# Kernel optimization log

Hardware: AMD Instinct MI355X
Metric: run time of the kernel (lower is better)

Reference implementation:

```python
import jax, jax.numpy as jnp
import numpy as np

EPS = 1e-5

def _conv1x1(x, w):
    # x: (B, Cin, N, K), w: (Cout, Cin) -> (B, Cout, N, K)
    return jnp.einsum('oc,bcnk->bonk', w, x)

def _bn2d(x, gamma, beta):
    # eval-mode BN with running_mean=0, running_var=1 (fresh init)
    scale = gamma / jnp.sqrt(1.0 + EPS)
    return x * scale[None, :, None, None] + beta[None, :, None, None]

def setup_inputs() -> dict:
    key = jax.random.key(0)
    ks = jax.random.split(key, 10)
    B, Cin, N, K = 8, 64, 1024, 32
    Cout, M = 64, 8
    Cin2 = 2 * Cin  # kernel_input='w_neighbor'
    features = jax.random.normal(ks[0], (B, Cin, N, K), dtype=jnp.float32)
    points_xyz = jax.random.normal(ks[1], (B, 3, N, K), dtype=jnp.float32)
    # ScoreNet convs: mlp_channels [7,16,16,16,M]; first 3 have BN (no bias), last has bias
    w1 = jax.random.normal(ks[2], (16, 7), dtype=jnp.float32) * (2.0 / 7) ** 0.5
    w2 = jax.random.normal(ks[3], (16, 16), dtype=jnp.float32) * (2.0 / 16) ** 0.5
    w3 = jax.random.normal(ks[4], (16, 16), dtype=jnp.float32) * (2.0 / 16) ** 0.5
    w4 = jax.random.normal(ks[5], (M, 16), dtype=jnp.float32) * (2.0 / 16) ** 0.5
    b4 = jnp.zeros((M,), dtype=jnp.float32)
    g1 = jnp.ones((16,), jnp.float32); be1 = jnp.zeros((16,), jnp.float32)
    g2 = jnp.ones((16,), jnp.float32); be2 = jnp.zeros((16,), jnp.float32)
    g3 = jnp.ones((16,), jnp.float32); be3 = jnp.zeros((16,), jnp.float32)
    # weight bank: kaiming_normal on (M, 2Cin, Cout) -> stored as (2Cin, M, Cout)
    wb = jax.random.normal(ks[6], (Cin2, M, Cout), dtype=jnp.float32) * (2.0 / Cin2) ** 0.5
    bn_g = jnp.ones((Cout,), jnp.float32); bn_b = jnp.zeros((Cout,), jnp.float32)
    return dict(features=features, points_xyz=points_xyz,
                w1=w1, g1=g1, be1=be1, w2=w2, g2=g2, be2=be2,
                w3=w3, g3=g3, be3=be3, w4=w4, b4=b4,
                weight_bank=wb, bn_g=bn_g, bn_b=bn_b)

def reference(features, points_xyz, w1, g1, be1, w2, g2, be2, w3, g3, be3,
              w4, b4, weight_bank, bn_g, bn_b):
    B, Cin, N, K = features.shape
    M = weight_bank.shape[1]
    # kernel_input = 'w_neighbor': concat(feat - center, feat) -> (B, 2Cin, N, K)
    center_f = features[..., :1]
    feat = jnp.concatenate([features - center_f, features], axis=1)
    # scorenet input = 'w_neighbor_dist': (center_xyz, xyz_diff, dist) -> (B, 7, N, K)
    center_xyz = jnp.broadcast_to(points_xyz[..., :1], points_xyz.shape)
    xyz_diff = points_xyz - center_xyz
    dist = jnp.sqrt(jnp.sum(xyz_diff * xyz_diff, axis=1, keepdims=True))
    xyz_feats = jnp.concatenate([center_xyz, xyz_diff, dist], axis=1)
    h = jax.nn.relu(_bn2d(_conv1x1(xyz_feats, w1), g1, be1))
    h = jax.nn.relu(_bn2d(_conv1x1(h, w2), g2, be2))
    h = jax.nn.relu(_bn2d(_conv1x1(h, w3), g3, be3))
    s = _conv1x1(h, w4) + b4[None, :, None, None]  # (B, M, N, K)
    scores = jax.nn.softmax(s, axis=1)
    scores = jnp.transpose(scores, (0, 2, 3, 1))  # (B, N, K, M)
    # matmul with weight bank then score-weighted sum over kernels, fused via einsum
    # original: (B,N,K,2Cin)@(2Cin,M*Cout) -> (B,N,K,M,Cout); sum_m scores * . -> (B,N,K,Cout)
    new_features = jnp.einsum('bcnk,cmo,bnkm->bonk', feat, weight_bank, scores)
    # BN2d (eval, fresh stats) + ReLU
    new_features = jax.nn.relu(_bn2d(new_features, bn_g, bn_b))
    return new_features
```

## Files before the change

### kernel.cpp

```cpp
#include <hip/hip_runtime.h>
#include <hip/hip_bf16.h>

typedef __attribute__((ext_vector_type(8))) short bf16x8;
typedef __attribute__((ext_vector_type(4))) float f32x4;
typedef __attribute__((ext_vector_type(2))) float f32x2;

#define BNSCL 0.9999950000375f

__global__ __launch_bounds__(256) void k_prep_wbt(const float* __restrict__ wb,
                                                  __hip_bfloat16* __restrict__ wbt)
{
    int idx = blockIdx.x * 256 + threadIdx.x;
    int o = idx >> 10;
    int cm = idx & 1023;
    wbt[idx] = __float2bfloat16(wb[cm * 64 + o]);
}

__global__ __launch_bounds__(256) void k_scores(
    const float* __restrict__ xyz,
    const float* __restrict__ w1, const float* __restrict__ g1, const float* __restrict__ be1,
    const float* __restrict__ w2, const float* __restrict__ g2, const float* __restrict__ be2,
    const float* __restrict__ w3, const float* __restrict__ g3, const float* __restrict__ be3,
    const float* __restrict__ w4, const float* __restrict__ b4,
    float* __restrict__ scores)
{
    __shared__ float lw[856];
    const int tid = threadIdx.x;
    if (tid < 112) lw[tid] = w1[tid];
    lw[112 + tid] = w2[tid];
    lw[368 + tid] = w3[tid];
    if (tid < 128) lw[624 + tid] = w4[tid];
    if (tid < 8)   lw[752 + tid] = b4[tid];
    if (tid < 16) {
        lw[760 + tid] = g1[tid] * BNSCL;  lw[776 + tid] = be1[tid];
        lw[792 + tid] = g2[tid] * BNSCL;  lw[808 + tid] = be2[tid];
        lw[824 + tid] = g3[tid] * BNSCL;  lw[840 + tid] = be3[tid];
    }
    __syncthreads();

    float in7[2][7], h1[2][16], h2[2][16], s[2][8];

#pragma unroll
    for (int q = 0; q < 2; ++q) {
        int g = blockIdx.x * 512 + q * 256 + tid;
        int b = g >> 15;
        int p = g & 32767;
        int pc = p & ~31;
        const float* xb = xyz + (size_t)b * 98304;
        float cx = xb[pc], cy = xb[32768 + pc], cz = xb[65536 + pc];
        float dx = xb[p] - cx, dy = xb[32768 + p] - cy, dz = xb[65536 + p] - cz;
        in7[q][0] = cx; in7[q][1] = cy; in7[q][2] = cz;
        in7[q][3] = dx; in7[q][4] = dy; in7[q][5] = dz;
        in7[q][6] = sqrtf(dx * dx + dy * dy + dz * dz);
    }

#pragma unroll
    for (int o = 0; o < 16; ++o) {
        float a0 = 0.f, a1 = 0.f;
#pragma unroll
        for (int c = 0; c < 7; ++c) {
            float w = lw[o * 7 + c];
            a0 += w * in7[0][c]; a1 += w * in7[1][c];
        }
        float gs = lw[760 + o], bb = lw[776 + o];
        h1[0][o] = fmaxf(a0 * gs + bb, 0.f);
        h1[1][o] = fmaxf(a1 * gs + bb, 0.f);
    }
#pragma unroll
    for (int o = 0; o < 16; ++o) {
        float a0 = 0.f, a1 = 0.f;
#pragma unroll
        for (int c = 0; c < 16; ++c) {
            float w = lw[112 + o * 16 + c];
            a0 += w * h1[0][c]; a1 += w * h1[1][c];
        }
        float gs = lw[792 + o], bb = lw[808 + o];
        h2[0][o] = fmaxf(a0 * gs + bb, 0.f);
        h2[1][o] = fmaxf(a1 * gs + bb, 0.f);
    }
#pragma unroll
    for (int o = 0; o < 16; ++o) {
        float a0 = 0.f, a1 = 0.f;
#pragma unroll
        for (int c = 0; c < 16; ++c) {
            float w = lw[368 + o * 16 + c];
            a0 += w * h2[0][c]; a1 += w * h2[1][c];
        }
        float gs = lw[824 + o], bb = lw[840 + o];
        h1[0][o] = fmaxf(a0 * gs + bb, 0.f);
        h1[1][o] = fmaxf(a1 * gs + bb, 0.f);
    }
#pragma unroll
    for (int o = 0; o < 8; ++o) {
        float bb = lw[752 + o];
        float a0 = bb, a1 = bb;
#pragma unroll
        for (int c = 0; c < 16; ++c) {
            float w = lw[624 + o * 16 + c];
            a0 += w * h1[0][c]; a1 += w * h1[1][c];
        }
        s[0][o] = a0; s[1][o] = a1;
    }

#pragma unroll
    for (int q = 0; q < 2; ++q) {
        int g = blockIdx.x * 512 + q * 256 + tid;
        float mx = s[q][0];
#pragma unroll
        for (int i = 1; i < 8; ++i) mx = fmaxf(mx, s[q][i]);
        float sum = 0.f;
#pragma unroll
        for (int i = 0; i < 8; ++i) { s[q][i] = __expf(s[q][i] - mx); sum += s[q][i]; }
        float inv = 1.f / sum;
        float4 lo = {s[q][0] * inv, s[q][1] * inv, s[q][2] * inv, s[q][3] * inv};
        float4 hi = {s[q][4] * inv, s[q][5] * inv, s[q][6] * inv, s[q][7] * inv};
        *(float4*)(scores + (size_t)g * 8) = lo;
        *(float4*)(scores + (size_t)g * 8 + 4) = hi;
    }
}

__global__ __launch_bounds__(512, 8) void k_main(
    const float* __restrict__ feat,
    const float* __restrict__ scores,
    const __hip_bfloat16* __restrict__ wbt,
    const float* __restrict__ bn_g, const float* __restrict__ bn_b,
    float* __restrict__ out)
{
    __shared__ __align__(16) short lwb[64 * 256];

    const int tid  = threadIdx.x;
    const int lane = tid & 63;
    const int wave = tid >> 6;
    const int col  = lane & 15;
    const int row4 = lane >> 4;

    const int pblock = blockIdx.x * 128;
    const int b    = pblock >> 15;
    const int pl0  = pblock & 32767;
    const int pcol = pl0 + wave * 16 + col;
    const int pcen = __builtin_amdgcn_readfirstlane(pcol & ~31);
    const int gp   = pblock + wave * 16 + col;

    const float* fb = feat + (size_t)b * 2097152;

    const float* sp = scores + (size_t)gp * 8;
    f32x2 s01 = *(const f32x2*)sp;
    f32x2 s23 = *(const f32x2*)(sp + 2);
    f32x2 s45 = *(const f32x2*)(sp + 4);
    f32x2 s67 = *(const f32x2*)(sp + 6);

    f32x4 acc[4];
#pragma unroll
    for (int i = 0; i < 4; ++i) { f32x4 z = {0.f, 0.f, 0.f, 0.f}; acc[i] = z; }

    const ushort* wsrc = (const ushort*)wbt;

#pragma unroll
    for (int phase = 0; phase < 4; ++phase) {
#pragma unroll
        for (int it = 0; it < 4; ++it) {
            int chunk = it * 512 + tid;
            int o = chunk >> 5, c8 = chunk & 31;
            int4 v = *(const int4*)(wsrc + (o << 10) + (phase << 8) + (c8 << 3));
            *(int4*)&lwb[(o << 8) + (((c8 ^ o) & 31) << 3)] = v;
        }
        __syncthreads();

#pragma unroll 4
        for (int kk = 0; kk < 8; ++kk) {
            int cp = phase * 32 + kk * 4 + row4;
            float fv;
            if (phase < 2) {
                const float* fpc = fb + (size_t)cp * 32768;
                fv = fpc[pcol] - fpc[pcen];
            } else {
                fv = fb[(size_t)(cp - 64) * 32768 + pcol];
            }

            f32x2 fvv = {fv, fv};
            f32x2 p0 = fvv * s01, p1 = fvv * s23, p2 = fvv * s45, p3 = fvv * s67;
            int4 bi;
            { __hip_bfloat162 q = __float22bfloat162_rn(make_float2(p0.x, p0.y)); __builtin_memcpy(&bi.x, &q, 4); }
            { __hip_bfloat162 q = __float22bfloat162_rn(make_float2(p1.x, p1.y)); __builtin_memcpy(&bi.y, &q, 4); }
            { __hip_bfloat162 q = __float22bfloat162_rn(make_float2(p2.x, p2.y)); __builtin_memcpy(&bi.z, &q, 4); }
            { __hip_bfloat162 q = __float22bfloat162_rn(make_float2(p3.x, p3.y)); __builtin_memcpy(&bi.w, &q, 4); }
            bf16x8 bv = __builtin_bit_cast(bf16x8, bi);

            int bcm = kk * 4 + row4;
#pragma unroll
            for (int ot = 0; ot < 4; ++ot) {
                int o = ot * 16 + col;
                bf16x8 af = *(const bf16x8*)&lwb[(o << 8) + (((bcm ^ o) & 31) << 3)];
                acc[ot] = __builtin_amdgcn_mfma_f32_16x16x32_bf16(af, bv, acc[ot], 0, 0, 0);
            }
        }
        __syncthreads();
    }

#pragma unroll
    for (int ot = 0; ot < 4; ++ot) {
#pragma unroll
        for (int r = 0; r < 4; ++r) {
            int o = ot * 16 + row4 * 4 + r;
            float v = acc[ot][r];
            v = v * (bn_g[o] * BNSCL) + bn_b[o];
            v = fmaxf(v, 0.f);
            out[((size_t)(b * 64 + o) << 15) + pcol] = v;
        }
    }
}

extern "C" void kernel_launch(void* const* d_in, const int* in_sizes, int n_in,
                              void* d_out, int out_size, void* d_ws, size_t ws_size,
                              hipStream_t stream)
{
    const float* features = (const float*)d_in[0];
    const float* xyz      = (const float*)d_in[1];
    const float* w1  = (const float*)d_in[2];
    const float* g1  = (const float*)d_in[3];
    const float* be1 = (const float*)d_in[4];
    const float* w2  = (const float*)d_in[5];
    const float* g2  = (const float*)d_in[6];
    const float* be2 = (const float*)d_in[7];
    const float* w3  = (const float*)d_in[8];
    const float* g3  = (const float*)d_in[9];
    const float* be3 = (const float*)d_in[10];
    const float* w4  = (const float*)d_in[11];
    const float* b4  = (const float*)d_in[12];
    const float* wb  = (const float*)d_in[13];
    const float* bn_g = (const float*)d_in[14];
    const float* bn_b = (const float*)d_in[15];

    float* scores = (float*)d_ws;
    __hip_bfloat16* wbt = (__hip_bfloat16*)((char*)d_ws + 8388608);

    k_prep_wbt<<<256, 256, 0, stream>>>(wb, wbt);
    k_scores<<<512, 256, 0, stream>>>(xyz, w1, g1, be1, w2, g2, be2,
                                      w3, g3, be3, w4, b4, scores);
    k_main<<<2048, 512, 0, stream>>>(features, scores, wbt, bn_g, bn_b,
                                     (float*)d_out);
}
```

Before: 199.0 us.

## Switch main GEMM to 32x32x16 MFMA with two point tiles per wave; fuse weight prep

```diff
diff --git a/kernel.cpp b/kernel.cpp
--- a/kernel.cpp
+++ b/kernel.cpp
@@ -2,19 +2,9 @@
 #include <hip/hip_bf16.h>
 
 typedef __attribute__((ext_vector_type(8))) short bf16x8;
-typedef __attribute__((ext_vector_type(4))) float f32x4;
-typedef __attribute__((ext_vector_type(2))) float f32x2;
+typedef __attribute__((ext_vector_type(16))) float f32x16;
 
 #define BNSCL 0.9999950000375f
-
-__global__ __launch_bounds__(256) void k_prep_wbt(const float* __restrict__ wb,
-                                                  __hip_bfloat16* __restrict__ wbt)
-{
-    int idx = blockIdx.x * 256 + threadIdx.x;
-    int o = idx >> 10;
-    int cm = idx & 1023;
-    wbt[idx] = __float2bfloat16(wb[cm * 64 + o]);
-}
 
 __global__ __launch_bounds__(256) void k_scores(
     const float* __restrict__ xyz,
@@ -22,10 +12,18 @@
     const float* __restrict__ w2, const float* __restrict__ g2, const float* __restrict__ be2,
     const float* __restrict__ w3, const float* __restrict__ g3, const float* __restrict__ be3,
     const float* __restrict__ w4, const float* __restrict__ b4,
+    const float* __restrict__ wb, __hip_bfloat16* __restrict__ wbt,
     float* __restrict__ scores)
 {
     __shared__ float lw[856];
     const int tid = threadIdx.x;
+
+    if (blockIdx.x < 256) {
+        int idx = blockIdx.x * 256 + tid;
+        int o = idx >> 10, cm = idx & 1023;
+        wbt[idx] = __float2bfloat16(wb[cm * 64 + o]);
+    }
+
     if (tid < 112) lw[tid] = w1[tid];
     lw[112 + tid] = w2[tid];
     lw[368 + tid] = w3[tid];
@@ -119,7 +117,7 @@
     }
 }
 
-__global__ __launch_bounds__(512, 8) void k_main(
+__global__ __launch_bounds__(256, 4) void k_main(
     const float* __restrict__ feat,
     const float* __restrict__ scores,
     const __hip_bfloat16* __restrict__ wbt,
@@ -131,81 +129,97 @@
     const int tid  = threadIdx.x;
     const int lane = tid & 63;
     const int wave = tid >> 6;
-    const int col  = lane & 15;
-    const int row4 = lane >> 4;
-
-    const int pblock = blockIdx.x * 128;
+    const int l31  = lane & 31;
+    const int lh   = lane >> 5;
+
+    const int pblock = blockIdx.x * 256;
     const int b    = pblock >> 15;
     const int pl0  = pblock & 32767;
-    const int pcol = pl0 + wave * 16 + col;
-    const int pcen = __builtin_amdgcn_readfirstlane(pcol & ~31);
-    const int gp   = pblock + wave * 16 + col;
+
+    const int ptl0 = pl0 + (wave * 2 + 0) * 32;
+    const int ptl1 = pl0 + (wave * 2 + 1) * 32;
+    const int pc0  = ptl0 + l31;
+    const int pc1  = ptl1 + l31;
 
     const float* fb = feat + (size_t)b * 2097152;
 
-    const float* sp = scores + (size_t)gp * 8;
-    f32x2 s01 = *(const f32x2*)sp;
-    f32x2 s23 = *(const f32x2*)(sp + 2);
-    f32x2 s45 = *(const f32x2*)(sp + 4);
-    f32x2 s67 = *(const f32x2*)(sp + 6);
-
-    f32x4 acc[4];
-#pragma unroll
-    for (int i = 0; i < 4; ++i) { f32x4 z = {0.f, 0.f, 0.f, 0.f}; acc[i] = z; }
+    const float* sp0 = scores + ((size_t)(pblock + (wave * 2) * 32 + l31)) * 8;
+    const float* sp1 = sp0 + 256;
+    float4 s0lo = *(const float4*)sp0, s0hi = *(const float4*)(sp0 + 4);
+    float4 s1lo = *(const float4*)sp1, s1hi = *(const float4*)(sp1 + 4);
+
+    f32x16 acc[2][2];
+#pragma unroll
+    for (int q = 0; q < 2; ++q)
+#pragma unroll
+        for (int ot = 0; ot < 2; ++ot) {
+            f32x16 z = {0.f,0.f,0.f,0.f,0.f,0.f,0.f,0.f,0.f,0.f,0.f,0.f,0.f,0.f,0.f,0.f};
+            acc[q][ot] = z;
+        }
 
     const ushort* wsrc = (const ushort*)wbt;
 
 #pragma unroll
     for (int phase = 0; phase < 4; ++phase) {
 #pragma unroll
-        for (int it = 0; it < 4; ++it) {
-            int chunk = it * 512 + tid;
+        for (int it = 0; it < 8; ++it) {
+            int chunk = it * 256 + tid;
             int o = chunk >> 5, c8 = chunk & 31;
             int4 v = *(const int4*)(wsrc + (o << 10) + (phase << 8) + (c8 << 3));
-            *(int4*)&lwb[(o << 8) + (((c8 ^ o) & 31) << 3)] = v;
+            *(int4*)&lwb[(o << 8) + (((c8 ^ (o & 31)) & 31) << 3)] = v;
         }
         __syncthreads();
 
 #pragma unroll 4
-        for (int kk = 0; kk < 8; ++kk) {
-            int cp = phase * 32 + kk * 4 + row4;
-            float fv;
+        for (int kk = 0; kk < 16; ++kk) {
+            int cr = ((phase & 1) << 5) + kk * 2 + lh;
+            const float* fr = fb + ((size_t)cr << 15);
+            float fv0, fv1;
             if (phase < 2) {
-                const float* fpc = fb + (size_t)cp * 32768;
-                fv = fpc[pcol] - fpc[pcen];
+                fv0 = fr[pc0] - fr[ptl0];
+                fv1 = fr[pc1] - fr[ptl1];
             } else {
-                fv = fb[(size_t)(cp - 64) * 32768 + pcol];
+                fv0 = fr[pc0];
+                fv1 = fr[pc1];
             }
 
-            f32x2 fvv = {fv, fv};
-            f32x2 p0 = fvv * s01, p1 = fvv * s23, p2 = fvv * s45, p3 = fvv * s67;
-            int4 bi;
-            { __hip_bfloat162 q = __float22bfloat162_rn(make_float2(p0.x, p0.y)); __builtin_memcpy(&bi.x, &q, 4); }
-            { __hip_bfloat162 q = __float22bfloat162_rn(make_float2(p1.x, p1.y)); __builtin_memcpy(&bi.y, &q, 4); }
-            { __hip_bfloat162 q = __float22bfloat162_rn(make_float2(p2.x, p2.y)); __builtin_memcpy(&bi.z, &q, 4); }
-            { __hip_bfloat162 q = __float22bfloat162_rn(make_float2(p3.x, p3.y)); __builtin_memcpy(&bi.w, &q, 4); }
-            bf16x8 bv = __builtin_bit_cast(bf16x8, bi);
-
-            int bcm = kk * 4 + row4;
-#pragma unroll
-            for (int ot = 0; ot < 4; ++ot) {
-                int o = ot * 16 + col;
-                bf16x8 af = *(const bf16x8*)&lwb[(o << 8) + (((bcm ^ o) & 31) << 3)];
-                acc[ot] = __builtin_amdgcn_mfma_f32_16x16x32_bf16(af, bv, acc[ot], 0, 0, 0);
+            int4 bi0, bi1;
+            { __hip_bfloat162 t = __float22bfloat162_rn(make_float2(fv0*s0lo.x, fv0*s0lo.y)); __builtin_memcpy(&bi0.x, &t, 4); }
+            { __hip_bfloat162 t = __float22bfloat162_rn(make_float2(fv0*s0lo.z, fv0*s0lo.w)); __builtin_memcpy(&bi0.y, &t, 4); }
+            { __hip_bfloat162 t = __float22bfloat162_rn(make_float2(fv0*s0hi.x, fv0*s0hi.y)); __builtin_memcpy(&bi0.z, &t, 4); }
+            { __hip_bfloat162 t = __float22bfloat162_rn(make_float2(fv0*s0hi.z, fv0*s0hi.w)); __builtin_memcpy(&bi0.w, &t, 4); }
+            { __hip_bfloat162 t = __float22bfloat162_rn(make_float2(fv1*s1lo.x, fv1*s1lo.y)); __builtin_memcpy(&bi1.x, &t, 4); }
+            { __hip_bfloat162 t = __float22bfloat162_rn(make_float2(fv1*s1lo.z, fv1*s1lo.w)); __builtin_memcpy(&bi1.y, &t, 4); }
+            { __hip_bfloat162 t = __float22bfloat162_rn(make_float2(fv1*s1hi.x, fv1*s1hi.y)); __builtin_memcpy(&bi1.z, &t, 4); }
+            { __hip_bfloat162 t = __float22bfloat162_rn(make_float2(fv1*s1hi.z, fv1*s1hi.w)); __builtin_memcpy(&bi1.w, &t, 4); }
+            bf16x8 bv0 = __builtin_bit_cast(bf16x8, bi0);
+            bf16x8 bv1 = __builtin_bit_cast(bf16x8, bi1);
+
+            int swz = ((kk * 2 + lh) ^ l31) & 31;
+#pragma unroll
+            for (int ot = 0; ot < 2; ++ot) {
+                int o = ot * 32 + l31;
+                bf16x8 af = *(const bf16x8*)&lwb[(o << 8) + (swz << 3)];
+                acc[0][ot] = __builtin_amdgcn_mfma_f32_32x32x16_bf16(af, bv0, acc[0][ot], 0, 0, 0);
+                acc[1][ot] = __builtin_amdgcn_mfma_f32_32x32x16_bf16(af, bv1, acc[1][ot], 0, 0, 0);
             }
         }
         __syncthreads();
     }
 
 #pragma unroll
-    for (int ot = 0; ot < 4; ++ot) {
-#pragma unroll
-        for (int r = 0; r < 4; ++r) {
-            int o = ot * 16 + row4 * 4 + r;
-            float v = acc[ot][r];
-            v = v * (bn_g[o] * BNSCL) + bn_b[o];
-            v = fmaxf(v, 0.f);
-            out[((size_t)(b * 64 + o) << 15) + pcol] = v;
+    for (int q = 0; q < 2; ++q) {
+        int pcol = (q == 0) ? pc0 : pc1;
+#pragma unroll
+        for (int ot = 0; ot < 2; ++ot) {
+#pragma unroll
+            for (int r = 0; r < 16; ++r) {
+                int o = ot * 32 + (r & 3) + ((r >> 2) << 3) + (lh << 2);
+                float v = acc[q][ot][r];
+                v = v * (bn_g[o] * BNSCL) + bn_b[o];
+                v = fmaxf(v, 0.f);
+                out[((size_t)(b * 64 + o) << 15) + pcol] = v;
+            }
         }
     }
 }
@@ -234,9 +248,8 @@
     float* scores = (float*)d_ws;
     __hip_bfloat16* wbt = (__hip_bfloat16*)((char*)d_ws + 8388608);
 
-    k_prep_wbt<<<256, 256, 0, stream>>>(wb, wbt);
     k_scores<<<512, 256, 0, stream>>>(xyz, w1, g1, be1, w2, g2, be2,
-                                      w3, g3, be3, w4, b4, scores);
-    k_main<<<2048, 512, 0, stream>>>(features, scores, wbt, bn_g, bn_b,
+                                      w3, g3, be3, w4, b4, wb, wbt, scores);
+    k_main<<<1024, 256, 0, stream>>>(features, scores, wbt, bn_g, bn_b,
                                      (float*)d_out);
 }
```

Measured after the change: 229.3 us. +15.2%, slower.
